# Kernel optimization log

Hardware: AMD Instinct MI355X
Metric: run time of the kernel (lower is better)

## Reference

```python
import math
import jax, jax.numpy as jnp
import numpy as np

S = 2048
D_MOD = 1024
D_K = 64
D_V = 64
H = 16
MASKED = True


def setup_inputs() -> dict:
    key = jax.random.key(0)
    ks = jax.random.split(key, 11)
    sc_in = 1.0 / math.sqrt(D_MOD)
    sc_o = 1.0 / math.sqrt(H * D_V)
    return {
        "Q_input": jax.random.normal(ks[0], (S, D_MOD), jnp.float32),
        "K_input": jax.random.normal(ks[1], (S, D_MOD), jnp.float32),
        "V_input": jax.random.normal(ks[2], (S, D_MOD), jnp.float32),
        # stacked per-head Linear params (torch Linear: y = x @ W.T + b)
        "WQw": jax.random.uniform(ks[3], (H, D_K, D_MOD), jnp.float32, -sc_in, sc_in),
        "WQb": jax.random.uniform(ks[4], (H, D_K), jnp.float32, -sc_in, sc_in),
        "WKw": jax.random.uniform(ks[5], (H, D_K, D_MOD), jnp.float32, -sc_in, sc_in),
        "WKb": jax.random.uniform(ks[6], (H, D_K), jnp.float32, -sc_in, sc_in),
        "WVw": jax.random.uniform(ks[7], (H, D_V, D_MOD), jnp.float32, -sc_in, sc_in),
        "WVb": jax.random.uniform(ks[8], (H, D_V), jnp.float32, -sc_in, sc_in),
        "WOw": jax.random.uniform(ks[9], (D_MOD, H * D_V), jnp.float32, -sc_o, sc_o),
        "WOb": jax.random.uniform(ks[10], (D_MOD,), jnp.float32, -sc_o, sc_o),
    }


def reference(Q_input, K_input, V_input, WQw, WQb, WKw, WKb, WVw, WVb, WOw, WOb):
    # per-head projections, batched over heads: [H, S, d]
    q = jnp.einsum("sd,hkd->hsk", Q_input, WQw) + WQb[:, None, :]
    k = jnp.einsum("sd,hkd->hsk", K_input, WKw) + WKb[:, None, :]
    v = jnp.einsum("sd,hvd->hsv", V_input, WVw) + WVb[:, None, :]
    # raw scores [H, S, T]
    qk = jnp.einsum("hsk,htk->hst", q, k)
    if MASKED:
        qk = jnp.tril(qk)  # torch.tril: zero (not -inf) upper triangle
    # torch log_softmax(dim=0) on each [S, T] matrix -> axis 1 of [H, S, T]
    scores = jax.nn.log_softmax(qk / math.sqrt(D_K), axis=1)
    attn = jnp.einsum("hst,htv->hsv", scores, v)  # [H, S, d_v]
    # torch.cat(head_attns, dim=1) -> [S, H*d_v], head-major feature order
    Z = jnp.transpose(attn, (1, 0, 2)).reshape(S, H * D_V)
    return Z @ WOw.T + WOb
```

## Files before the change

### kernel.cpp

```cpp
#include <hip/hip_runtime.h>
#include <math.h>
#include <stdint.h>

#define S 2048
#define DMOD 1024
#define H 16

typedef unsigned short ushort_t;
typedef short bf16x8 __attribute__((ext_vector_type(8)));
typedef float f32x4 __attribute__((ext_vector_type(4)));

#define SW(r) ((((r) & 7)) ^ ((((r) >> 3) & 3) << 1))

__device__ __forceinline__ ushort_t f2b(float f) {
    union { float f; unsigned u; } x; x.f = f;
    return (ushort_t)((x.u + 0x7FFFu + ((x.u >> 16) & 1u)) >> 16);
}
__device__ __forceinline__ float b2f(ushort_t b) {
    union { unsigned u; float f; } x; x.u = ((unsigned)b) << 16;
    return x.f;
}
__device__ __forceinline__ void gld16(const ushort_t* g, ushort_t* l) {
    __builtin_amdgcn_global_load_lds(
        (const __attribute__((address_space(1))) unsigned int*)g,
        (__attribute__((address_space(3))) unsigned int*)l, 16, 0, 0);
}

__global__ void init_sumexp(float* __restrict__ sumexp) {
    int i = blockIdx.x * blockDim.x + threadIdx.x;
    if (i < H * S)               sumexp[i] = (float)(i & (S - 1));
    else if (i < H * S + H * 64) sumexp[i] = 0.f;
}

__global__ __launch_bounds__(256) void convert_all(
    const float* q, const float* k, const float* v,
    const float* wq, const float* wk, const float* wv, const float* wo,
    ushort_t* qo, ushort_t* ko, ushort_t* vo,
    ushort_t* wqo, ushort_t* wko, ushort_t* wvo, ushort_t* woo)
{
    const int seg = blockIdx.y;
    const float* src; ushort_t* dst; size_t off = 0;
    const size_t M1 = (size_t)1 << 20;
    if (seg < 2)       { src = q;  dst = qo;  off = (size_t)seg * M1; }
    else if (seg < 4)  { src = k;  dst = ko;  off = (size_t)(seg - 2) * M1; }
    else if (seg < 6)  { src = v;  dst = vo;  off = (size_t)(seg - 4) * M1; }
    else if (seg == 6) { src = wq; dst = wqo; }
    else if (seg == 7) { src = wk; dst = wko; }
    else if (seg == 8) { src = wv; dst = wvo; }
    else               { src = wo; dst = woo; }
    size_t i = off + ((size_t)blockIdx.x * 256 + threadIdx.x) * 4;
    float4 f = *(const float4*)(src + i);
    union { uint2 u2; ushort_t us[4]; } o;
    o.us[0] = f2b(f.x); o.us[1] = f2b(f.y); o.us[2] = f2b(f.z); o.us[3] = f2b(f.w);
    *(uint2*)(dst + i) = o.u2;
}

__global__ __launch_bounds__(256) void gemm_qkv(
    const ushort_t* __restrict__ A0, const ushort_t* __restrict__ A1,
    const ushort_t* __restrict__ A2, const ushort_t* __restrict__ Wqkv,
    const float* __restrict__ b0, const float* __restrict__ b1,
    const float* __restrict__ b2,
    ushort_t* __restrict__ qbb, ushort_t* __restrict__ kbb,
    ushort_t* __restrict__ vt)
{
    __shared__ ushort_t As[128 * 64];
    __shared__ ushort_t Bs[64 * 64];
    const int tid = threadIdx.x;
    const int lane = tid & 63, wid = tid >> 6;
    const int quad = lane >> 4, l15 = lane & 15;
    const int wr = wid >> 1, wc = wid & 1;
    const int m0 = blockIdx.y * 128;
    const int n0 = blockIdx.x * 64;
    const int seg = n0 >> 10;
    const int nloc = n0 & 1023;
    const ushort_t* A = seg == 0 ? A0 : (seg == 1 ? A1 : A2);
    const float* bias = seg == 0 ? b0 : (seg == 1 ? b1 : b2);

    const f32x4 fz = {0.f, 0.f, 0.f, 0.f};
    f32x4 acc[4][2];
#pragma unroll
    for (int i = 0; i < 4; ++i) { acc[i][0] = fz; acc[i][1] = fz; }

    for (int k0 = 0; k0 < DMOD; k0 += 64) {
        __syncthreads();
#pragma unroll
        for (int i = 0; i < 4; ++i) {
            int c = i * 256 + tid, row = c >> 3, kcl = c & 7;
            gld16(A + (size_t)(m0 + row) * DMOD + k0 + (kcl ^ SW(row)) * 8, &As[c * 8]);
        }
#pragma unroll
        for (int i = 0; i < 2; ++i) {
            int c = i * 256 + tid, row = c >> 3, kcl = c & 7;
            gld16(Wqkv + (size_t)(n0 + row) * DMOD + k0 + (kcl ^ SW(row)) * 8, &Bs[c * 8]);
        }
        __syncthreads();
#pragma unroll
        for (int kc = 0; kc < 2; ++kc) {
            bf16x8 af[4], bfr[2];
#pragma unroll
            for (int mi = 0; mi < 4; ++mi) {
                int row = wr * 64 + mi * 16 + l15;
                af[mi] = *(const bf16x8*)&As[row * 64 + ((kc * 4 + quad) ^ SW(row)) * 8];
            }
#pragma unroll
            for (int ni = 0; ni < 2; ++ni) {
                int row = wc * 32 + ni * 16 + l15;
                bfr[ni] = *(const bf16x8*)&Bs[row * 64 + ((kc * 4 + quad) ^ SW(row)) * 8];
            }
#pragma unroll
            for (int mi = 0; mi < 4; ++mi)
#pragma unroll
                for (int ni = 0; ni < 2; ++ni)
                    acc[mi][ni] = __builtin_amdgcn_mfma_f32_16x16x32_bf16(
                        af[mi], bfr[ni], acc[mi][ni], 0, 0, 0);
        }
    }

    if (seg < 2) {
        ushort_t* C = seg == 0 ? qbb : kbb;
#pragma unroll
        for (int mi = 0; mi < 4; ++mi)
#pragma unroll
            for (int ni = 0; ni < 2; ++ni) {
                int gn = nloc + wc * 32 + ni * 16 + l15;
                float bv = bias[gn];
#pragma unroll
                for (int r = 0; r < 4; ++r) {
                    int gm = m0 + wr * 64 + mi * 16 + quad * 4 + r;
                    C[(size_t)gm * DMOD + gn] = f2b(acc[mi][ni][r] + bv);
                }
            }
    } else {
#pragma unroll
        for (int mi = 0; mi < 4; ++mi)
#pragma unroll
            for (int ni = 0; ni < 2; ++ni) {
                int gn = nloc + wc * 32 + ni * 16 + l15;
                float bv = bias[gn];
                int gmb = m0 + wr * 64 + mi * 16 + quad * 4;
                union { uint2 u2; ushort_t us[4]; } o;
#pragma unroll
                for (int r = 0; r < 4; ++r) o.us[r] = f2b(acc[mi][ni][r] + bv);
                *(uint2*)&vt[(size_t)gn * S + gmb] = o.u2;
            }
    }
}

__global__ __launch_bounds__(256) void attn_mfma(
    const ushort_t* __restrict__ qb, const ushort_t* __restrict__ kb,
    const ushort_t* __restrict__ vt, float* __restrict__ attn_raw,
    float* __restrict__ sumexp)
{
    __shared__ ushort_t Qs[4096];
    __shared__ ushort_t Ks[2][4096];
    __shared__ ushort_t Vs[2][4096];
    __shared__ ushort_t Ps[4096];

    const int h = blockIdx.y;
    const int bx = blockIdx.x;
    const int si = 31 - (bx >> 1);
    const int z = bx & 1;
    const int nt = si + 1;
    const int half0 = (nt + 1) >> 1;
    const int tbeg = z ? half0 : 0;
    const int tend = z ? nt : half0;
    if (tbeg >= tend) return;
    const int s0 = si * 64;

    const int tid = threadIdx.x;
    const int lane = tid & 63, w = tid >> 6;
    const int quad = lane >> 4, l15 = lane & 15;

    const ushort_t* qh = qb + h * 64;
    const ushort_t* kh = kb + h * 64;
    const ushort_t* vh = vt + (size_t)(h * 64) * S;

#pragma unroll
    for (int i = 0; i < 2; ++i) {
        int c = i * 256 + tid, row = c >> 3, kcl = c & 7;
        gld16(qh + (size_t)(s0 + row) * DMOD + (kcl ^ SW(row)) * 8, &Qs[c * 8]);
    }
    {
        int t0 = tbeg * 64;
#pragma unroll
        for (int i = 0; i < 2; ++i) {
            int c = i * 256 + tid, row = c >> 3, kcl = c & 7;
            gld16(kh + (size_t)(t0 + row) * DMOD + (kcl ^ SW(row)) * 8, &Ks[0][c * 8]);
            gld16(vh + (size_t)row * S + t0 + (kcl ^ SW(row)) * 8, &Vs[0][c * 8]);
        }
    }
    __syncthreads();

    const f32x4 fz = {0.f, 0.f, 0.f, 0.f};
    f32x4 oacc[4];
#pragma unroll
    for (int ni = 0; ni < 4; ++ni) oacc[ni] = fz;

    for (int it = tbeg; it < tend; ++it) {
        const int p = (it - tbeg) & 1;
        const int t0 = it * 64;
        if (it + 1 < tend) {
            int t1 = t0 + 64;
#pragma unroll
            for (int i = 0; i < 2; ++i) {
                int c = i * 256 + tid, row = c >> 3, kcl = c & 7;
                gld16(kh + (size_t)(t1 + row) * DMOD + (kcl ^ SW(row)) * 8, &Ks[1 - p][c * 8]);
                gld16(vh + (size_t)row * S + t1 + (kcl ^ SW(row)) * 8, &Vs[1 - p][c * 8]);
            }
        }

        f32x4 xf[4];
#pragma unroll
        for (int ti = 0; ti < 4; ++ti) xf[ti] = fz;
#pragma unroll
        for (int kc = 0; kc < 2; ++kc) {
            int rq = w * 16 + l15;
            bf16x8 aq = *(const bf16x8*)&Qs[rq * 64 + ((kc * 4 + quad) ^ SW(rq)) * 8];
#pragma unroll
            for (int ti = 0; ti < 4; ++ti) {
                int rk = ti * 16 + l15;
                bf16x8 bk = *(const bf16x8*)&Ks[p][rk * 64 + ((kc * 4 + quad) ^ SW(rk)) * 8];
                xf[ti] = __builtin_amdgcn_mfma_f32_16x16x32_bf16(aq, bk, xf[ti], 0, 0, 0);
            }
        }

        const int s_base = s0 + w * 16 + quad * 4;
        const bool diag = (t0 == s0);
#pragma unroll
        for (int ti = 0; ti < 4; ++ti) {
            int t_g = t0 + ti * 16 + l15;
            float es = 0.f;
#pragma unroll
            for (int r = 0; r < 4; ++r) {
                float xv = xf[ti][r] * 0.125f;
                bool live = (!diag) || (s_base + r >= t_g);
                xv = live ? xv : 0.f;
                es += live ? __expf(xv) : 0.f;
                xf[ti][r] = xv;
            }
            es += __shfl_xor(es, 16, 64);
            es += __shfl_xor(es, 32, 64);
            if (quad == 0) atomicAdd(&sumexp[h * S + t_g], es);
#pragma unroll
            for (int r = 0; r < 4; ++r) {
                int sl = w * 16 + quad * 4 + r;
                int tc = ti * 16 + l15;
                Ps[sl * 64 + ((tc >> 3) ^ SW(sl)) * 8 + (tc & 7)] = f2b(xf[ti][r]);
            }
        }

#pragma unroll
        for (int kc = 0; kc < 2; ++kc) {
            int rp = w * 16 + l15;
            bf16x8 ap = *(const bf16x8*)&Ps[rp * 64 + ((kc * 4 + quad) ^ SW(rp)) * 8];
#pragma unroll
            for (int ni = 0; ni < 4; ++ni) {
                int rv = ni * 16 + l15;
                bf16x8 bv = *(const bf16x8*)&Vs[p][rv * 64 + ((kc * 4 + quad) ^ SW(rv)) * 8];
                oacc[ni] = __builtin_amdgcn_mfma_f32_16x16x32_bf16(ap, bv, oacc[ni], 0, 0, 0);
            }
        }
        __syncthreads();
    }

#pragma unroll
    for (int ni = 0; ni < 4; ++ni)
#pragma unroll
        for (int r = 0; r < 4; ++r) {
            int s_g = s0 + w * 16 + quad * 4 + r;
            atomicAdd(&attn_raw[(size_t)s_g * DMOD + h * 64 + ni * 16 + l15],
                      oacc[ni][r]);
        }
}

__global__ void lse_kernel(float* __restrict__ sumexp) {
    int i = blockIdx.x * blockDim.x + threadIdx.x;
    if (i < H * S) sumexp[i] = logf(sumexp[i]);
}

__global__ __launch_bounds__(256) void corr_kernel(
    const float* __restrict__ lse, const ushort_t* __restrict__ vt,
    float* __restrict__ corr)
{
    const int w = threadIdx.x >> 6, lane = threadIdx.x & 63;
    const int r = blockIdx.x * 4 + w;
    const int h = r >> 6;
    float acc = 0.f;
#pragma unroll
    for (int i = 0; i < 4; ++i) {
        int t = i * 512 + lane * 8;
        bf16x8 vv = *(const bf16x8*)&vt[(size_t)r * S + t];
        float4 l0 = *(const float4*)&lse[h * S + t];
        float4 l1 = *(const float4*)&lse[h * S + t + 4];
        acc += l0.x * b2f((ushort_t)vv[0]) + l0.y * b2f((ushort_t)vv[1])
             + l0.z * b2f((ushort_t)vv[2]) + l0.w * b2f((ushort_t)vv[3])
             + l1.x * b2f((ushort_t)vv[4]) + l1.y * b2f((ushort_t)vv[5])
             + l1.z * b2f((ushort_t)vv[6]) + l1.w * b2f((ushort_t)vv[7]);
    }
#pragma unroll
    for (int d = 1; d < 64; d <<= 1) acc += __shfl_xor(acc, d, 64);
    if (lane == 0) corr[r] = acc;
}

__global__ __launch_bounds__(256) void convert_Z(
    const float* __restrict__ attn_raw, const float* __restrict__ corr,
    ushort_t* __restrict__ Zb)
{
    size_t i = ((size_t)blockIdx.x * 256 + threadIdx.x) * 4;
    float4 f = *(const float4*)(attn_raw + i);
    int c = (int)(i & (DMOD - 1));
    union { uint2 u2; ushort_t us[4]; } o;
    o.us[0] = f2b(f.x - corr[c]);
    o.us[1] = f2b(f.y - corr[c + 1]);
    o.us[2] = f2b(f.z - corr[c + 2]);
    o.us[3] = f2b(f.w - corr[c + 3]);
    *(uint2*)(Zb + i) = o.u2;
}

__global__ __launch_bounds__(256) void gemm_out(
    const ushort_t* __restrict__ A, const ushort_t* __restrict__ W,
    const float* __restrict__ bias, float* __restrict__ C)
{
    __shared__ ushort_t As[128 * 64];
    __shared__ ushort_t Bs[64 * 64];
    const int tid = threadIdx.x;
    const int lane = tid & 63, wid = tid >> 6;
    const int quad = lane >> 4, l15 = lane & 15;
    const int wr = wid >> 1, wc = wid & 1;
    const int m0 = blockIdx.y * 128, n0 = blockIdx.x * 64;
    const int kbeg = blockIdx.z * 512, kend = kbeg + 512;

    const f32x4 fz = {0.f, 0.f, 0.f, 0.f};
    f32x4 acc[4][2];
#pragma unroll
    for (int i = 0; i < 4; ++i) { acc[i][0] = fz; acc[i][1] = fz; }

    for (int k0 = kbeg; k0 < kend; k0 += 64) {
        __syncthreads();
#pragma unroll
        for (int i = 0; i < 4; ++i) {
            int c = i * 256 + tid, row = c >> 3, kcl = c & 7;
            gld16(A + (size_t)(m0 + row) * DMOD + k0 + (kcl ^ SW(row)) * 8, &As[c * 8]);
        }
#pragma unroll
        for (int i = 0; i < 2; ++i) {
            int c = i * 256 + tid, row = c >> 3, kcl = c & 7;
            gld16(W + (size_t)(n0 + row) * DMOD + k0 + (kcl ^ SW(row)) * 8, &Bs[c * 8]);
        }
        __syncthreads();
#pragma unroll
        for (int kc = 0; kc < 2; ++kc) {
            bf16x8 af[4], bfr[2];
#pragma unroll
            for (int mi = 0; mi < 4; ++mi) {
                int row = wr * 64 + mi * 16 + l15;
                af[mi] = *(const bf16x8*)&As[row * 64 + ((kc * 4 + quad) ^ SW(row)) * 8];
            }
#pragma unroll
            for (int ni = 0; ni < 2; ++ni) {
                int row = wc * 32 + ni * 16 + l15;
                bfr[ni] = *(const bf16x8*)&Bs[row * 64 + ((kc * 4 + quad) ^ SW(row)) * 8];
            }
#pragma unroll
            for (int mi = 0; mi < 4; ++mi)
#pragma unroll
                for (int ni = 0; ni < 2; ++ni)
                    acc[mi][ni] = __builtin_amdgcn_mfma_f32_16x16x32_bf16(
                        af[mi], bfr[ni], acc[mi][ni], 0, 0, 0);
        }
    }
#pragma unroll
    for (int mi = 0; mi < 4; ++mi)
#pragma unroll
        for (int ni = 0; ni < 2; ++ni) {
            int gn = n0 + wc * 32 + ni * 16 + l15;
            float bv = (kbeg == 0) ? bias[gn] : 0.f;
#pragma unroll
            for (int r = 0; r < 4; ++r) {
                int gm = m0 + wr * 64 + mi * 16 + quad * 4 + r;
                atomicAdd(&C[(size_t)gm * DMOD + gn], acc[mi][ni][r] + bv);
            }
        }
}

extern "C" void kernel_launch(void* const* d_in, const int* in_sizes, int n_in,
                              void* d_out, int out_size, void* d_ws, size_t ws_size,
                              hipStream_t stream) {
    const float* Qin = (const float*)d_in[0];
    const float* Kin = (const float*)d_in[1];
    const float* Vin = (const float*)d_in[2];
    const float* WQw = (const float*)d_in[3];
    const float* WQb = (const float*)d_in[4];
    const float* WKw = (const float*)d_in[5];
    const float* WKb = (const float*)d_in[6];
    const float* WVw = (const float*)d_in[7];
    const float* WVb = (const float*)d_in[8];
    const float* WOw = (const float*)d_in[9];
    const float* WOb = (const float*)d_in[10];

    float* ws = (float*)d_ws;
    const size_t M1 = (size_t)1 << 20;
    ushort_t* qbb  = (ushort_t*)(ws);
    ushort_t* kbb  = (ushort_t*)(ws + M1);
    ushort_t* vt   = (ushort_t*)(ws + 2 * M1);
    ushort_t* wqkv = (ushort_t*)(ws + 3 * M1);
    ushort_t* wob  = (ushort_t*)(ws + 4 * M1 + M1 / 2);
    ushort_t* Qbin = (ushort_t*)(ws + 5 * M1);
    ushort_t* Kbin = (ushort_t*)(ws + 6 * M1);
    ushort_t* Vbin = (ushort_t*)(ws + 7 * M1);
    float* attn_raw = ws + 6 * M1;
    ushort_t* Zb    = (ushort_t*)(ws + 5 * M1);
    float* sumexp   = ws + 8 * M1;
    float* corr     = ws + 8 * M1 + H * S;

    init_sumexp<<<(H * S + H * 64 + 255) / 256, 256, 0, stream>>>(sumexp);
    hipMemsetAsync(attn_raw, 0, (size_t)S * DMOD * sizeof(float), stream);
    hipMemsetAsync(d_out, 0, (size_t)S * DMOD * sizeof(float), stream);

    convert_all<<<dim3(1024, 10), 256, 0, stream>>>(
        Qin, Kin, Vin, WQw, WKw, WVw, WOw,
        Qbin, Kbin, Vbin,
        wqkv, wqkv + (size_t)1024 * 1024, wqkv + (size_t)2 * 1024 * 1024, wob);

    gemm_qkv<<<dim3(48, 16), 256, 0, stream>>>(
        Qbin, Kbin, Vbin, wqkv, WQb, WKb, WVb, qbb, kbb, vt);

    attn_mfma<<<dim3(64, H), 256, 0, stream>>>(qbb, kbb, vt, attn_raw, sumexp);

    lse_kernel<<<128, 256, 0, stream>>>(sumexp);
    corr_kernel<<<256, 256, 0, stream>>>(sumexp, vt, corr);
    convert_Z<<<2048, 256, 0, stream>>>(attn_raw, corr, Zb);

    gemm_out<<<dim3(16, 16, 2), 256, 0, stream>>>(Zb, wob, WOb, (float*)d_out);
}
```

Before: 214.3 us.

## Widen attention tiles to 128 query rows, batch sumexp atomics in LDS, fuse init kernels

The attention kernel now uses 512-thread blocks that each cover 128 query rows against shared 64-wide K/V tiles, which halves K/V loads per query row. Q fragments are hoisted into registers, and fully masked warp bands skip their MFMA work. Per-column exp sums go into a shared-memory accumulator and are flushed with one global atomic per column per block, cutting global atomic traffic. The init kernel and the two memsets are merged into one launch, and the log is folded into corr_kernel so lse_kernel is gone. In exchange the grid has fewer, larger blocks and more LDS per block, which may reduce occupancy.

```diff
diff --git a/kernel.cpp b/kernel.cpp
--- a/kernel.cpp
+++ b/kernel.cpp
@@ -26,10 +26,24 @@
         (__attribute__((address_space(3))) unsigned int*)l, 16, 0, 0);
 }
 
-__global__ void init_sumexp(float* __restrict__ sumexp) {
-    int i = blockIdx.x * blockDim.x + threadIdx.x;
-    if (i < H * S)               sumexp[i] = (float)(i & (S - 1));
-    else if (i < H * S + H * 64) sumexp[i] = 0.f;
+__global__ __launch_bounds__(256) void init_all(
+    float* __restrict__ attn_raw, float* __restrict__ out,
+    float* __restrict__ sumexp, float* __restrict__ corr)
+{
+    const int b = blockIdx.x;
+    const float4 z4 = {0.f, 0.f, 0.f, 0.f};
+    if (b < 2048) {
+        *(float4*)(attn_raw + ((size_t)b * 256 + threadIdx.x) * 4) = z4;
+    } else if (b < 4096) {
+        *(float4*)(out + ((size_t)(b - 2048) * 256 + threadIdx.x) * 4) = z4;
+    } else if (b < 4128) {
+        int e = ((b - 4096) * 256 + threadIdx.x) * 4;
+        float4 v = {(float)(e & 2047), (float)((e + 1) & 2047),
+                    (float)((e + 2) & 2047), (float)((e + 3) & 2047)};
+        *(float4*)(sumexp + e) = v;
+    } else {
+        *(float4*)(corr + threadIdx.x * 4) = z4;
+    }
 }
 
 __global__ __launch_bounds__(256) void convert_all(
@@ -146,30 +160,30 @@
     }
 }
 
-__global__ __launch_bounds__(256) void attn_mfma(
+__global__ __launch_bounds__(512, 4) void attn_mfma(
     const ushort_t* __restrict__ qb, const ushort_t* __restrict__ kb,
     const ushort_t* __restrict__ vt, float* __restrict__ attn_raw,
     float* __restrict__ sumexp)
 {
-    __shared__ ushort_t Qs[4096];
+    __shared__ ushort_t Qs[128 * 64];
     __shared__ ushort_t Ks[2][4096];
     __shared__ ushort_t Vs[2][4096];
-    __shared__ ushort_t Ps[4096];
+    __shared__ ushort_t Ps[128 * 64];
+    __shared__ float    sacc[1024];
 
     const int h = blockIdx.y;
     const int bx = blockIdx.x;
-    const int si = 31 - (bx >> 1);
+    const int si = 15 - (bx >> 1);
     const int z = bx & 1;
-    const int nt = si + 1;
-    const int half0 = (nt + 1) >> 1;
-    const int tbeg = z ? half0 : 0;
-    const int tend = z ? nt : half0;
-    if (tbeg >= tend) return;
-    const int s0 = si * 64;
+    const int half = si + 1;
+    const int tbeg = z ? half : 0;
+    const int tend = z ? 2 * si + 2 : half;
+    const int s0 = si * 128;
 
     const int tid = threadIdx.x;
     const int lane = tid & 63, w = tid >> 6;
     const int quad = lane >> 4, l15 = lane & 15;
+    const int sband = s0 + w * 16;
 
     const ushort_t* qh = qb + h * 64;
     const ushort_t* kh = kb + h * 64;
@@ -177,19 +191,25 @@
 
 #pragma unroll
     for (int i = 0; i < 2; ++i) {
-        int c = i * 256 + tid, row = c >> 3, kcl = c & 7;
+        int c = i * 512 + tid, row = c >> 3, kcl = c & 7;
         gld16(qh + (size_t)(s0 + row) * DMOD + (kcl ^ SW(row)) * 8, &Qs[c * 8]);
     }
     {
         int t0 = tbeg * 64;
-#pragma unroll
-        for (int i = 0; i < 2; ++i) {
-            int c = i * 256 + tid, row = c >> 3, kcl = c & 7;
-            gld16(kh + (size_t)(t0 + row) * DMOD + (kcl ^ SW(row)) * 8, &Ks[0][c * 8]);
-            gld16(vh + (size_t)row * S + t0 + (kcl ^ SW(row)) * 8, &Vs[0][c * 8]);
-        }
-    }
+        int row = tid >> 3, kcl = tid & 7;
+        gld16(kh + (size_t)(t0 + row) * DMOD + (kcl ^ SW(row)) * 8, &Ks[0][tid * 8]);
+        gld16(vh + (size_t)row * S + t0 + (kcl ^ SW(row)) * 8, &Vs[0][tid * 8]);
+    }
+    for (int i = tid; i < 1024; i += 512) sacc[i] = 0.f;
     __syncthreads();
+
+    bf16x8 aq[2];
+    {
+        int rq = w * 16 + l15;
+#pragma unroll
+        for (int kc = 0; kc < 2; ++kc)
+            aq[kc] = *(const bf16x8*)&Qs[rq * 64 + ((kc * 4 + quad) ^ SW(rq)) * 8];
+    }
 
     const f32x4 fz = {0.f, 0.f, 0.f, 0.f};
     f32x4 oacc[4];
@@ -201,68 +221,70 @@
         const int t0 = it * 64;
         if (it + 1 < tend) {
             int t1 = t0 + 64;
-#pragma unroll
-            for (int i = 0; i < 2; ++i) {
-                int c = i * 256 + tid, row = c >> 3, kcl = c & 7;
-                gld16(kh + (size_t)(t1 + row) * DMOD + (kcl ^ SW(row)) * 8, &Ks[1 - p][c * 8]);
-                gld16(vh + (size_t)row * S + t1 + (kcl ^ SW(row)) * 8, &Vs[1 - p][c * 8]);
-            }
-        }
-
-        f32x4 xf[4];
-#pragma unroll
-        for (int ti = 0; ti < 4; ++ti) xf[ti] = fz;
-#pragma unroll
-        for (int kc = 0; kc < 2; ++kc) {
-            int rq = w * 16 + l15;
-            bf16x8 aq = *(const bf16x8*)&Qs[rq * 64 + ((kc * 4 + quad) ^ SW(rq)) * 8];
+            int row = tid >> 3, kcl = tid & 7;
+            gld16(kh + (size_t)(t1 + row) * DMOD + (kcl ^ SW(row)) * 8, &Ks[1 - p][tid * 8]);
+            gld16(vh + (size_t)row * S + t1 + (kcl ^ SW(row)) * 8, &Vs[1 - p][tid * 8]);
+        }
+
+        if (t0 < sband + 16) {
+            f32x4 xf[4];
+#pragma unroll
+            for (int ti = 0; ti < 4; ++ti) xf[ti] = fz;
+#pragma unroll
+            for (int kc = 0; kc < 2; ++kc) {
+#pragma unroll
+                for (int ti = 0; ti < 4; ++ti) {
+                    int rk = ti * 16 + l15;
+                    bf16x8 bk = *(const bf16x8*)&Ks[p][rk * 64 + ((kc * 4 + quad) ^ SW(rk)) * 8];
+                    xf[ti] = __builtin_amdgcn_mfma_f32_16x16x32_bf16(aq[kc], bk, xf[ti], 0, 0, 0);
+                }
+            }
+
+            const bool clean = (t0 + 63 <= sband);
+            const int s_q = sband + quad * 4;
 #pragma unroll
             for (int ti = 0; ti < 4; ++ti) {
-                int rk = ti * 16 + l15;
-                bf16x8 bk = *(const bf16x8*)&Ks[p][rk * 64 + ((kc * 4 + quad) ^ SW(rk)) * 8];
-                xf[ti] = __builtin_amdgcn_mfma_f32_16x16x32_bf16(aq, bk, xf[ti], 0, 0, 0);
-            }
-        }
-
-        const int s_base = s0 + w * 16 + quad * 4;
-        const bool diag = (t0 == s0);
-#pragma unroll
-        for (int ti = 0; ti < 4; ++ti) {
-            int t_g = t0 + ti * 16 + l15;
-            float es = 0.f;
-#pragma unroll
-            for (int r = 0; r < 4; ++r) {
-                float xv = xf[ti][r] * 0.125f;
-                bool live = (!diag) || (s_base + r >= t_g);
-                xv = live ? xv : 0.f;
-                es += live ? __expf(xv) : 0.f;
-                xf[ti][r] = xv;
-            }
-            es += __shfl_xor(es, 16, 64);
-            es += __shfl_xor(es, 32, 64);
-            if (quad == 0) atomicAdd(&sumexp[h * S + t_g], es);
-#pragma unroll
-            for (int r = 0; r < 4; ++r) {
-                int sl = w * 16 + quad * 4 + r;
-                int tc = ti * 16 + l15;
-                Ps[sl * 64 + ((tc >> 3) ^ SW(sl)) * 8 + (tc & 7)] = f2b(xf[ti][r]);
-            }
-        }
-
-#pragma unroll
-        for (int kc = 0; kc < 2; ++kc) {
-            int rp = w * 16 + l15;
-            bf16x8 ap = *(const bf16x8*)&Ps[rp * 64 + ((kc * 4 + quad) ^ SW(rp)) * 8];
-#pragma unroll
-            for (int ni = 0; ni < 4; ++ni) {
-                int rv = ni * 16 + l15;
-                bf16x8 bv = *(const bf16x8*)&Vs[p][rv * 64 + ((kc * 4 + quad) ^ SW(rv)) * 8];
-                oacc[ni] = __builtin_amdgcn_mfma_f32_16x16x32_bf16(ap, bv, oacc[ni], 0, 0, 0);
+                int t_g = t0 + ti * 16 + l15;
+                float es = 0.f;
+#pragma unroll
+                for (int r = 0; r < 4; ++r) {
+                    float xv = xf[ti][r] * 0.125f;
+                    bool live = clean || (s_q + r >= t_g);
+                    xv = live ? xv : 0.f;
+                    es += live ? __expf(xv) : 0.f;
+                    xf[ti][r] = xv;
+                }
+                es += __shfl_xor(es, 16, 64);
+                es += __shfl_xor(es, 32, 64);
+                if (quad == 0) atomicAdd(&sacc[t0 - tbeg * 64 + ti * 16 + l15], es);
+#pragma unroll
+                for (int r = 0; r < 4; ++r) {
+                    int sl = w * 16 + quad * 4 + r;
+                    int tc = ti * 16 + l15;
+                    Ps[sl * 64 + ((tc >> 3) ^ SW(sl)) * 8 + (tc & 7)] = f2b(xf[ti][r]);
+                }
+            }
+
+#pragma unroll
+            for (int kc = 0; kc < 2; ++kc) {
+                int rp = w * 16 + l15;
+                bf16x8 ap = *(const bf16x8*)&Ps[rp * 64 + ((kc * 4 + quad) ^ SW(rp)) * 8];
+#pragma unroll
+                for (int ni = 0; ni < 4; ++ni) {
+                    int rv = ni * 16 + l15;
+                    bf16x8 bv = *(const bf16x8*)&Vs[p][rv * 64 + ((kc * 4 + quad) ^ SW(rv)) * 8];
+                    oacc[ni] = __builtin_amdgcn_mfma_f32_16x16x32_bf16(ap, bv, oacc[ni], 0, 0, 0);
+                }
             }
         }
         __syncthreads();
     }
 
+    {
+        int nv = (tend - tbeg) * 64;
+        for (int i = tid; i < nv; i += 512)
+            atomicAdd(&sumexp[h * S + tbeg * 64 + i], sacc[i]);
+    }
 #pragma unroll
     for (int ni = 0; ni < 4; ++ni)
 #pragma unroll
@@ -273,13 +295,8 @@
         }
 }
 
-__global__ void lse_kernel(float* __restrict__ sumexp) {
-    int i = blockIdx.x * blockDim.x + threadIdx.x;
-    if (i < H * S) sumexp[i] = logf(sumexp[i]);
-}
-
 __global__ __launch_bounds__(256) void corr_kernel(
-    const float* __restrict__ lse, const ushort_t* __restrict__ vt,
+    const float* __restrict__ sumexp, const ushort_t* __restrict__ vt,
     float* __restrict__ corr)
 {
     const int w = threadIdx.x >> 6, lane = threadIdx.x & 63;
@@ -290,12 +307,12 @@
     for (int i = 0; i < 4; ++i) {
         int t = i * 512 + lane * 8;
         bf16x8 vv = *(const bf16x8*)&vt[(size_t)r * S + t];
-        float4 l0 = *(const float4*)&lse[h * S + t];
-        float4 l1 = *(const float4*)&lse[h * S + t + 4];
-        acc += l0.x * b2f((ushort_t)vv[0]) + l0.y * b2f((ushort_t)vv[1])
-             + l0.z * b2f((ushort_t)vv[2]) + l0.w * b2f((ushort_t)vv[3])
-             + l1.x * b2f((ushort_t)vv[4]) + l1.y * b2f((ushort_t)vv[5])
-             + l1.z * b2f((ushort_t)vv[6]) + l1.w * b2f((ushort_t)vv[7]);
+        float4 s0 = *(const float4*)&sumexp[h * S + t];
+        float4 s1 = *(const float4*)&sumexp[h * S + t + 4];
+        acc += logf(s0.x) * b2f((ushort_t)vv[0]) + logf(s0.y) * b2f((ushort_t)vv[1])
+             + logf(s0.z) * b2f((ushort_t)vv[2]) + logf(s0.w) * b2f((ushort_t)vv[3])
+             + logf(s1.x) * b2f((ushort_t)vv[4]) + logf(s1.y) * b2f((ushort_t)vv[5])
+             + logf(s1.z) * b2f((ushort_t)vv[6]) + logf(s1.w) * b2f((ushort_t)vv[7]);
     }
 #pragma unroll
     for (int d = 1; d < 64; d <<= 1) acc += __shfl_xor(acc, d, 64);
@@ -413,9 +430,7 @@
     float* sumexp   = ws + 8 * M1;
     float* corr     = ws + 8 * M1 + H * S;
 
-    init_sumexp<<<(H * S + H * 64 + 255) / 256, 256, 0, stream>>>(sumexp);
-    hipMemsetAsync(attn_raw, 0, (size_t)S * DMOD * sizeof(float), stream);
-    hipMemsetAsync(d_out, 0, (size_t)S * DMOD * sizeof(float), stream);
+    init_all<<<4129, 256, 0, stream>>>(attn_raw, (float*)d_out, sumexp, corr);
 
     convert_all<<<dim3(1024, 10), 256, 0, stream>>>(
         Qin, Kin, Vin, WQw, WKw, WVw, WOw,
@@ -425,9 +440,8 @@
     gemm_qkv<<<dim3(48, 16), 256, 0, stream>>>(
         Qbin, Kbin, Vbin, wqkv, WQb, WKb, WVb, qbb, kbb, vt);
 
-    attn_mfma<<<dim3(64, H), 256, 0, stream>>>(qbb, kbb, vt, attn_raw, sumexp);
-
-    lse_kernel<<<128, 256, 0, stream>>>(sumexp);
+    attn_mfma<<<dim3(32, H), 512, 0, stream>>>(qbb, kbb, vt, attn_raw, sumexp);
+
     corr_kernel<<<256, 256, 0, stream>>>(sumexp, vt, corr);
     convert_Z<<<2048, 256, 0, stream>>>(attn_raw, corr, Zb);
 
```

After: 204.7 us. -4.5%, faster.
